# Optimization experiments

Measured on AMD Instinct MI355X. Metric: run time of the kernel, lower is better.

## Reference

```python
import jax, jax.numpy as jnp
import numpy as np

INPUT_SIZE = 2048
HIDDEN_SIZE = 2048
BATCH = 4096


def setup_inputs() -> dict:
    key = jax.random.key(0)
    ks = jax.random.split(key, 16)
    s_in = 1.0 / np.sqrt(INPUT_SIZE)
    s_h = 1.0 / np.sqrt(HIDDEN_SIZE)
    d = {
        "x": jax.random.normal(ks[0], (BATCH, INPUT_SIZE), jnp.float32),
        "h": jax.random.normal(ks[1], (BATCH, HIDDEN_SIZE), jnp.float32),
        "c": jax.random.normal(ks[2], (BATCH, HIDDEN_SIZE), jnp.float32),
    }
    # input-side weights [H, I] and biases (torch nn.Linear layout)
    for i, g in enumerate(["f", "i", "c", "o"]):
        d[f"W{g}x"] = jax.random.uniform(ks[3 + i], (HIDDEN_SIZE, INPUT_SIZE), jnp.float32, -s_in, s_in)
        d[f"b{g}x"] = jax.random.uniform(ks[7 + i], (HIDDEN_SIZE,), jnp.float32, -s_in, s_in)
        d[f"W{g}h"] = jax.random.uniform(ks[11 + i], (HIDDEN_SIZE, HIDDEN_SIZE), jnp.float32, -s_h, s_h)
    return d


def reference(x, h, c, Wfx, bfx, Wfh, Wix, bix, Wih, Wcx, bcx, Wch, Wox, box, Woh):
    # gate pre-activations: x @ W*x.T + b + h @ W*h.T
    f = jax.nn.relu(x @ Wfx.T + bfx + h @ Wfh.T)
    i = jax.nn.relu(x @ Wix.T + bix + h @ Wih.T)
    o = jax.nn.relu(x @ Wox.T + box + h @ Woh.T)
    c_tilde = jnp.tanh(x @ Wcx.T + bcx + h @ Wch.T)
    c_new = f * c + i * c_tilde
    h_new = o * jnp.tanh(c_new)
    return (h_new, c_new)
```

## Files before the change

kernel.cpp:

```cpp
#include <hip/hip_runtime.h>
#include <hip/hip_bf16.h>


#define HID 2048
#define BATCH_N 4096
#define KTOT 4096
#define BM 128
#define BN 64
#define BK 64
#define THREADS 256

typedef __attribute__((ext_vector_type(4))) float f32x4;
typedef __attribute__((ext_vector_type(8))) short bf16x8;

__device__ __forceinline__ short f2bf(float f) {
    union { float f; unsigned u; } v; v.f = f;
    unsigned r = v.u + 0x7FFFu + ((v.u >> 16) & 1u);
    return (short)(r >> 16);
}

__device__ __forceinline__ float fast_tanh(float v) {
    float e = __expf(2.0f * v);
    return 1.0f - 2.0f / (e + 1.0f);
}

__device__ __forceinline__ void gload_lds16(const short* g, short* l) {
    __builtin_amdgcn_global_load_lds(
        (const __attribute__((address_space(1))) unsigned int*)g,
        (__attribute__((address_space(3))) unsigned int*)l, 16, 0, 0);
}

struct CastParams {
    const float* x; const float* h;
    const float* Wx[4]; const float* Wh[4];
    short* A; short* B;
};

__global__ __launch_bounds__(256) void precast_kernel(CastParams q) {
    const long A_CH = (long)BATCH_N * (KTOT / 8);
    const long B_CH = 4L * HID * (KTOT / 8);
    const long total = A_CH + B_CH;
    for (long idx = (long)blockIdx.x * 256 + threadIdx.x; idx < total;
         idx += (long)gridDim.x * 256) {
        const float* src; short* dst; int row, k;
        if (idx < A_CH) {
            row = (int)(idx >> 9);
            k = (int)(idx & 511) << 3;
            src = (k < HID) ? &q.x[(size_t)row * HID + k]
                            : &q.h[(size_t)row * HID + (k - HID)];
            dst = &q.A[(size_t)row * KTOT];
        } else {
            long r = idx - A_CH;
            int g = (int)(r >> 20);
            int rem = (int)(r & ((1 << 20) - 1));
            row = rem >> 9;
            k = (rem & 511) << 3;
            src = (k < HID) ? &q.Wx[g][(size_t)row * HID + k]
                            : &q.Wh[g][(size_t)row * HID + (k - HID)];
            dst = &q.B[((size_t)g * HID + row) * KTOT];
        }
        float4 v0 = *(const float4*)src;
        float4 v1 = *(const float4*)(src + 4);
        int col = (k & ~63) | ((k & 63) ^ ((row & 7) << 3));
        bf16x8 s;
        s[0] = f2bf(v0.x); s[1] = f2bf(v0.y); s[2] = f2bf(v0.z); s[3] = f2bf(v0.w);
        s[4] = f2bf(v1.x); s[5] = f2bf(v1.y); s[6] = f2bf(v1.z); s[7] = f2bf(v1.w);
        *(bf16x8*)&dst[col] = s;
    }
}

struct GemmParams {
    const short* A; const short* B;
    const float* bx[4];
    const float* c;
    float* oh; float* oc;
};

__global__ __launch_bounds__(THREADS, 2) void gemm_lstm_kernel(GemmParams p) {
    __shared__ short sA[BM * BK];
    __shared__ short sB[4 * BN * BK];

    const int t = threadIdx.x;
    const int bm = blockIdx.x * BM;
    const int bn = blockIdx.y * BN;
    const int wave = t >> 6;
    const int lane = t & 63;
    const int wm = (wave >> 1) * 64;
    const int wn = (wave & 1) * 32;
    const int lr = lane & 15;
    const int lk = (lane >> 4) * 8;

    f32x4 acc[4][4][2];
    #pragma unroll
    for (int g = 0; g < 4; ++g)
        #pragma unroll
        for (int m = 0; m < 4; ++m)
            #pragma unroll
            for (int n = 0; n < 2; ++n)
                acc[g][m][n] = (f32x4){0.f, 0.f, 0.f, 0.f};

    const int srow = lane >> 3;
    const int kch = (lane & 7) * 8;
    const short* gA = p.A + (size_t)(bm + wave * 32 + srow) * KTOT + kch;
    const short* gB = p.B + ((size_t)wave * HID + bn + srow) * KTOT + kch;

    for (int k0 = 0; k0 < KTOT; k0 += BK) {
        #pragma unroll
        for (int j = 0; j < 4; ++j)
            gload_lds16(gA + (size_t)(j * 8) * KTOT + k0,
                        &sA[(wave * 32 + j * 8) * BK]);
        #pragma unroll
        for (int j = 0; j < 8; ++j)
            gload_lds16(gB + (size_t)(j * 8) * KTOT + k0,
                        &sB[(wave * 64 + j * 8) * BK]);

        __syncthreads();

        #pragma unroll
        for (int kk = 0; kk < 2; ++kk) {
            bf16x8 a[4];
            #pragma unroll
            for (int m = 0; m < 4; ++m) {
                int row = wm + m * 16 + lr;
                int kidx = (kk * 32 + lk) ^ ((row & 7) << 3);
                a[m] = *(const bf16x8*)&sA[row * BK + kidx];
            }
            #pragma unroll
            for (int g = 0; g < 4; ++g) {
                #pragma unroll
                for (int n = 0; n < 2; ++n) {
                    int brow = wn + n * 16 + lr;
                    int kidx = (kk * 32 + lk) ^ ((brow & 7) << 3);
                    bf16x8 b = *(const bf16x8*)&sB[(g * BN + brow) * BK + kidx];
                    #pragma unroll
                    for (int m = 0; m < 4; ++m)
                        acc[g][m][n] = __builtin_amdgcn_mfma_f32_16x16x32_bf16(
                            a[m], b, acc[g][m][n], 0, 0, 0);
                }
            }
        }

        __syncthreads();
    }

    float bias[4][2];
    #pragma unroll
    for (int g = 0; g < 4; ++g)
        #pragma unroll
        for (int n = 0; n < 2; ++n)
            bias[g][n] = p.bx[g][bn + wn + n * 16 + lr];

    #pragma unroll
    for (int m = 0; m < 4; ++m) {
        int rbase = bm + wm + m * 16 + (lane >> 4) * 4;
        #pragma unroll
        for (int r = 0; r < 4; ++r) {
            int row = rbase + r;
            #pragma unroll
            for (int n = 0; n < 2; ++n) {
                int col = bn + wn + n * 16 + lr;
                float pf = acc[0][m][n][r] + bias[0][n];
                float pi = acc[1][m][n][r] + bias[1][n];
                float pc = acc[2][m][n][r] + bias[2][n];
                float po = acc[3][m][n][r] + bias[3][n];
                float fg = fmaxf(pf, 0.f);
                float ig = fmaxf(pi, 0.f);
                float og = fmaxf(po, 0.f);
                float ct = fast_tanh(pc);
                float cv = p.c[(size_t)row * HID + col];
                float cn = fg * cv + ig * ct;
                float hn = og * fast_tanh(cn);
                p.oh[(size_t)row * HID + col] = hn;
                p.oc[(size_t)row * HID + col] = cn;
            }
        }
    }
}

struct Params {
    const float* x; const float* h; const float* c;
    const float* Wx[4]; const float* Wh[4]; const float* bx[4];
    float* oh; float* oc;
};

__global__ __launch_bounds__(THREADS, 2) void relulstm_fallback(Params p) {
    __shared__ short sA[BM * BK];
    __shared__ short sB[4][BN * BK];
    const int t = threadIdx.x;
    const int bm = blockIdx.x * BM;
    const int bn = blockIdx.y * BN;
    const int wave = t >> 6;
    const int lane = t & 63;
    const int wm = (wave >> 1) * 64;
    const int wn = (wave & 1) * 32;
    const int lr = lane & 15;
    const int lk = (lane >> 4) * 8;

    f32x4 acc[4][4][2];
    #pragma unroll
    for (int g = 0; g < 4; ++g)
        #pragma unroll
        for (int m = 0; m < 4; ++m)
            #pragma unroll
            for (int n = 0; n < 2; ++n)
                acc[g][m][n] = (f32x4){0.f, 0.f, 0.f, 0.f};

    for (int k0 = 0; k0 < 2 * HID; k0 += BK) {
        const bool xpart = (k0 < HID);
        const int kb = k0 & (HID - 1);
        const float* __restrict__ srcA = xpart ? p.x : p.h;
        #pragma unroll
        for (int i2 = 0; i2 < 8; ++i2) {
            int cidx = t + i2 * THREADS;
            int row = cidx >> 4;
            int kc = cidx & 15;
            float4 v = *(const float4*)&srcA[(size_t)(bm + row) * HID + kb + kc * 4];
            int idx = row * BK + ((kc * 4) ^ ((row & 7) << 3));
            short4 s;
            s.x = f2bf(v.x); s.y = f2bf(v.y); s.z = f2bf(v.z); s.w = f2bf(v.w);
            *(short4*)&sA[idx] = s;
        }
        #pragma unroll
        for (int i2 = 0; i2 < 16; ++i2) {
            const int g = i2 >> 2;
            int rem = t + (i2 & 3) * THREADS;
            int row = rem >> 4;
            int kc = rem & 15;
            const float* __restrict__ srcB = xpart ? p.Wx[g] : p.Wh[g];
            float4 v = *(const float4*)&srcB[(size_t)(bn + row) * HID + kb + kc * 4];
            int idx = row * BK + ((kc * 4) ^ ((row & 7) << 3));
            short4 s;
            s.x = f2bf(v.x); s.y = f2bf(v.y); s.z = f2bf(v.z); s.w = f2bf(v.w);
            *(short4*)&sB[g][idx] = s;
        }
        __syncthreads();
        #pragma unroll
        for (int kk = 0; kk < 2; ++kk) {
            bf16x8 a[4];
            #pragma unroll
            for (int m = 0; m < 4; ++m) {
                int row = wm + m * 16 + lr;
                int kidx = (kk * 32 + lk) ^ ((row & 7) << 3);
                a[m] = *(const bf16x8*)&sA[row * BK + kidx];
            }
            #pragma unroll
            for (int g = 0; g < 4; ++g) {
                #pragma unroll
                for (int n = 0; n < 2; ++n) {
                    int brow = wn + n * 16 + lr;
                    int kidx = (kk * 32 + lk) ^ ((brow & 7) << 3);
                    bf16x8 b = *(const bf16x8*)&sB[g][brow * BK + kidx];
                    #pragma unroll
                    for (int m = 0; m < 4; ++m)
                        acc[g][m][n] = __builtin_amdgcn_mfma_f32_16x16x32_bf16(
                            a[m], b, acc[g][m][n], 0, 0, 0);
                }
            }
        }
        __syncthreads();
    }

    float bias[4][2];
    #pragma unroll
    for (int g = 0; g < 4; ++g)
        #pragma unroll
        for (int n = 0; n < 2; ++n)
            bias[g][n] = p.bx[g][bn + wn + n * 16 + lr];

    #pragma unroll
    for (int m = 0; m < 4; ++m) {
        int rbase = bm + wm + m * 16 + (lane >> 4) * 4;
        #pragma unroll
        for (int r = 0; r < 4; ++r) {
            int row = rbase + r;
            #pragma unroll
            for (int n = 0; n < 2; ++n) {
                int col = bn + wn + n * 16 + lr;
                float pf = acc[0][m][n][r] + bias[0][n];
                float pi = acc[1][m][n][r] + bias[1][n];
                float pc = acc[2][m][n][r] + bias[2][n];
                float po = acc[3][m][n][r] + bias[3][n];
                float fg = fmaxf(pf, 0.f);
                float ig = fmaxf(pi, 0.f);
                float og = fmaxf(po, 0.f);
                float ct = fast_tanh(pc);
                float cv = p.c[(size_t)row * HID + col];
                float cn = fg * cv + ig * ct;
                float hn = og * fast_tanh(cn);
                p.oh[(size_t)row * HID + col] = hn;
                p.oc[(size_t)row * HID + col] = cn;
            }
        }
    }
}

extern "C" void kernel_launch(void* const* d_in, const int* in_sizes, int n_in,
                              void* d_out, int out_size, void* d_ws, size_t ws_size,
                              hipStream_t stream) {
    (void)in_sizes; (void)n_in; (void)out_size;
    const size_t A_BYTES = (size_t)BATCH_N * KTOT * 2;
    const size_t B_BYTES = (size_t)4 * HID * KTOT * 2;

    if (ws_size >= A_BYTES + B_BYTES) {
        short* A = (short*)d_ws;
        short* B = A + (size_t)BATCH_N * KTOT;

        CastParams q;
        q.x = (const float*)d_in[0];
        q.h = (const float*)d_in[1];
        for (int g = 0; g < 4; ++g) {
            q.Wx[g] = (const float*)d_in[3 + 3 * g];
            q.Wh[g] = (const float*)d_in[5 + 3 * g];
        }
        q.A = A; q.B = B;
        precast_kernel<<<2048, 256, 0, stream>>>(q);

        GemmParams p;
        p.A = A; p.B = B;
        p.c = (const float*)d_in[2];
        for (int g = 0; g < 4; ++g) p.bx[g] = (const float*)d_in[4 + 3 * g];
        p.oh = (float*)d_out;
        p.oc = (float*)d_out + (size_t)BATCH_N * HID;
        dim3 grid(BATCH_N / BM, HID / BN);
        gemm_lstm_kernel<<<grid, THREADS, 0, stream>>>(p);
    } else {
        Params p;
        p.x = (const float*)d_in[0];
        p.h = (const float*)d_in[1];
        p.c = (const float*)d_in[2];
        for (int g = 0; g < 4; ++g) {
            p.Wx[g] = (const float*)d_in[3 + 3 * g];
            p.bx[g] = (const float*)d_in[4 + 3 * g];
            p.Wh[g] = (const float*)d_in[5 + 3 * g];
        }
        p.oh = (float*)d_out;
        p.oc = (float*)d_out + (size_t)BATCH_N * HID;
        dim3 grid(BATCH_N / BM, HID / BN);
        relulstm_fallback<<<grid, THREADS, 0, stream>>>(p);
    }
}
```

Measured before the change: 318.9 us.

## Rewrite fused LSTM GEMM as 8-wave double-buffered, phase-interleaved pipeline

Replaces the 256-thread single-buffered GEMM with a 512-thread kernel computing a 256x64 tile per gate. LDS is double-buffered, and global-to-LDS loads for later K-chunks are interleaved across eight per-gate MFMA phases, with explicit vmcnt waits, barriers and setprio. The aim is to hide global load latency behind MFMA work and to reuse each B tile across more rows. In exchange it uses 64KB of LDS and carries high register pressure, which may limit occupancy, and the hand-scheduled barriers are fragile.

```diff
diff --git a/kernel.cpp b/kernel.cpp
--- a/kernel.cpp
+++ b/kernel.cpp
@@ -5,10 +5,7 @@
 #define HID 2048
 #define BATCH_N 4096
 #define KTOT 4096
-#define BM 128
-#define BN 64
 #define BK 64
-#define THREADS 256
 
 typedef __attribute__((ext_vector_type(4))) float f32x4;
 typedef __attribute__((ext_vector_type(8))) short bf16x8;
@@ -76,13 +73,157 @@
     float* oh; float* oc;
 };
 
-__global__ __launch_bounds__(THREADS, 2) void gemm_lstm_kernel(GemmParams p) {
-    __shared__ short sA[BM * BK];
-    __shared__ short sB[4 * BN * BK];
+__global__ __launch_bounds__(512, 2) void gemm_lstm_8ph(GemmParams p) {
+    __shared__ short sA[2][16384];
+    __shared__ short sB[2][16384];
 
     const int t = threadIdx.x;
-    const int bm = blockIdx.x * BM;
-    const int bn = blockIdx.y * BN;
+    const int wave = t >> 6;
+    const int lane = t & 63;
+    const int wr = wave >> 1;
+    const int wc = wave & 1;
+    const int lr = lane & 15;
+    const int lk = (lane >> 4) * 8;
+    const int sw = (lane & 7) << 3;
+    const int koff0 = lk ^ sw;
+    const int koff1 = (32 + lk) ^ sw;
+
+    const int bm = blockIdx.x * 256;
+    const int bn = blockIdx.y * 64;
+
+    const int aOff = (wr * 64 + lr) * 64;
+    const int bOff = (wc * 32 + lr) * 64;
+
+    const short* aSrc = p.A + (size_t)(bm + (t >> 3)) * KTOT + (t & 7) * 8;
+    const short* bSrc = p.B + (size_t)(bn + (t >> 3)) * KTOT + (t & 7) * 8;
+    const int ldsT = t * 8;
+
+    f32x4 acc[4][4][2];
+    #pragma unroll
+    for (int g = 0; g < 4; ++g)
+        #pragma unroll
+        for (int m = 0; m < 4; ++m)
+            #pragma unroll
+            for (int n = 0; n < 2; ++n)
+                acc[g][m][n] = (f32x4){0.f, 0.f, 0.f, 0.f};
+
+    bf16x8 a[4][2];
+    bf16x8 b[2][2];
+
+#define STAGE_A(bf, u, kp) gload_lds16(aSrc + (size_t)(u) * 64 * KTOT + (kp), \
+                                       &sA[bf][(u) * 4096 + ldsT])
+#define STAGE_B(bf, g, kp) gload_lds16(bSrc + (size_t)(g) * HID * KTOT + (kp), \
+                                       &sB[bf][(g) * 4096 + ldsT])
+#define READ_A(bf) do { _Pragma("unroll") for (int m = 0; m < 4; ++m) { \
+        a[m][0] = *(const bf16x8*)&sA[bf][aOff + m * 1024 + koff0]; \
+        a[m][1] = *(const bf16x8*)&sA[bf][aOff + m * 1024 + koff1]; } } while (0)
+#define READ_B(bf, g) do { _Pragma("unroll") for (int n = 0; n < 2; ++n) { \
+        b[n][0] = *(const bf16x8*)&sB[bf][(g) * 4096 + bOff + n * 1024 + koff0]; \
+        b[n][1] = *(const bf16x8*)&sB[bf][(g) * 4096 + bOff + n * 1024 + koff1]; } } while (0)
+#define MFMA_G(g) do { __builtin_amdgcn_s_setprio(1); \
+        _Pragma("unroll") for (int kk = 0; kk < 2; ++kk) \
+        _Pragma("unroll") for (int n = 0; n < 2; ++n) \
+        _Pragma("unroll") for (int m = 0; m < 4; ++m) \
+            acc[g][m][n] = __builtin_amdgcn_mfma_f32_16x16x32_bf16( \
+                a[m][kk], b[n][kk], acc[g][m][n], 0, 0, 0); \
+        __builtin_amdgcn_s_setprio(0); } while (0)
+#define BAR() __builtin_amdgcn_s_barrier()
+#define VMCNT6() asm volatile("s_waitcnt vmcnt(6)" ::: "memory")
+
+    STAGE_A(0, 0, 0); STAGE_A(0, 1, 0); STAGE_A(0, 2, 0); STAGE_A(0, 3, 0);
+    STAGE_B(0, 0, 0); STAGE_B(0, 1, 0); STAGE_B(0, 2, 0); STAGE_B(0, 3, 0);
+    STAGE_A(1, 0, BK); STAGE_A(1, 1, BK); STAGE_A(1, 2, BK); STAGE_A(1, 3, BK);
+    STAGE_B(1, 0, BK); STAGE_B(1, 1, BK);
+    VMCNT6();
+    BAR();
+
+    for (int it = 0; it < KTOT / (2 * BK); ++it) {
+        const int kc1 = ((2 * it + 1) * BK) & (KTOT - 1);
+        const int kc2 = ((2 * it + 2) * BK) & (KTOT - 1);
+        const int kc3 = ((2 * it + 3) * BK) & (KTOT - 1);
+
+        READ_A(0); READ_B(0, 0);
+        STAGE_B(1, 2, kc1); STAGE_B(1, 3, kc1);
+        BAR(); MFMA_G(0); BAR();
+        READ_B(0, 1);
+        STAGE_A(0, 0, kc2); STAGE_A(0, 1, kc2);
+        BAR(); MFMA_G(1); BAR();
+        READ_B(0, 2);
+        STAGE_A(0, 2, kc2); STAGE_A(0, 3, kc2);
+        BAR(); MFMA_G(2); BAR();
+        READ_B(0, 3);
+        STAGE_B(0, 0, kc2); STAGE_B(0, 1, kc2);
+        VMCNT6();
+        BAR(); MFMA_G(3); BAR();
+        READ_A(1); READ_B(1, 0);
+        STAGE_B(0, 2, kc2); STAGE_B(0, 3, kc2);
+        BAR(); MFMA_G(0); BAR();
+        READ_B(1, 1);
+        STAGE_A(1, 0, kc3); STAGE_A(1, 1, kc3);
+        BAR(); MFMA_G(1); BAR();
+        READ_B(1, 2);
+        STAGE_A(1, 2, kc3); STAGE_A(1, 3, kc3);
+        BAR(); MFMA_G(2); BAR();
+        READ_B(1, 3);
+        STAGE_B(1, 0, kc3); STAGE_B(1, 1, kc3);
+        VMCNT6();
+        BAR(); MFMA_G(3); BAR();
+    }
+    asm volatile("s_waitcnt vmcnt(0)" ::: "memory");
+
+    float bias[4][2];
+    #pragma unroll
+    for (int g = 0; g < 4; ++g)
+        #pragma unroll
+        for (int n = 0; n < 2; ++n)
+            bias[g][n] = p.bx[g][bn + wc * 32 + n * 16 + lr];
+
+    #pragma unroll
+    for (int m = 0; m < 4; ++m) {
+        int rbase = bm + wr * 64 + m * 16 + (lane >> 4) * 4;
+        #pragma unroll
+        for (int r = 0; r < 4; ++r) {
+            int row = rbase + r;
+            #pragma unroll
+            for (int n = 0; n < 2; ++n) {
+                int col = bn + wc * 32 + n * 16 + lr;
+                float pf = acc[0][m][n][r] + bias[0][n];
+                float pi = acc[1][m][n][r] + bias[1][n];
+                float pc = acc[2][m][n][r] + bias[2][n];
+                float po = acc[3][m][n][r] + bias[3][n];
+                float fg = fmaxf(pf, 0.f);
+                float ig = fmaxf(pi, 0.f);
+                float og = fmaxf(po, 0.f);
+                float ct = fast_tanh(pc);
+                float cv = p.c[(size_t)row * HID + col];
+                float cn = fg * cv + ig * ct;
+                float hn = og * fast_tanh(cn);
+                p.oh[(size_t)row * HID + col] = hn;
+                p.oc[(size_t)row * HID + col] = cn;
+            }
+        }
+    }
+#undef STAGE_A
+#undef STAGE_B
+#undef READ_A
+#undef READ_B
+#undef MFMA_G
+#undef BAR
+#undef VMCNT6
+}
+
+struct Params {
+    const float* x; const float* h; const float* c;
+    const float* Wx[4]; const float* Wh[4]; const float* bx[4];
+    float* oh; float* oc;
+};
+
+__global__ __launch_bounds__(256, 2) void relulstm_fallback(Params p) {
+    __shared__ short sA[128 * 64];
+    __shared__ short sB[4][64 * 64];
+    const int t = threadIdx.x;
+    const int bm = blockIdx.x * 128;
+    const int bn = blockIdx.y * 64;
     const int wave = t >> 6;
     const int lane = t & 63;
     const int wm = (wave >> 1) * 64;
@@ -99,23 +240,35 @@
             for (int n = 0; n < 2; ++n)
                 acc[g][m][n] = (f32x4){0.f, 0.f, 0.f, 0.f};
 
-    const int srow = lane >> 3;
-    const int kch = (lane & 7) * 8;
-    const short* gA = p.A + (size_t)(bm + wave * 32 + srow) * KTOT + kch;
-    const short* gB = p.B + ((size_t)wave * HID + bn + srow) * KTOT + kch;
-
-    for (int k0 = 0; k0 < KTOT; k0 += BK) {
-        #pragma unroll
-        for (int j = 0; j < 4; ++j)
-            gload_lds16(gA + (size_t)(j * 8) * KTOT + k0,
-                        &sA[(wave * 32 + j * 8) * BK]);
-        #pragma unroll
-        for (int j = 0; j < 8; ++j)
-            gload_lds16(gB + (size_t)(j * 8) * KTOT + k0,
-                        &sB[(wave * 64 + j * 8) * BK]);
-
+    for (int k0 = 0; k0 < 2 * HID; k0 += BK) {
+        const bool xpart = (k0 < HID);
+        const int kb = k0 & (HID - 1);
+        const float* __restrict__ srcA = xpart ? p.x : p.h;
+        #pragma unroll
+        for (int i2 = 0; i2 < 8; ++i2) {
+            int cidx = t + i2 * 256;
+            int row = cidx >> 4;
+            int kc = cidx & 15;
+            float4 v = *(const float4*)&srcA[(size_t)(bm + row) * HID + kb + kc * 4];
+            int idx = row * BK + ((kc * 4) ^ ((row & 7) << 3));
+            short4 s;
+            s.x = f2bf(v.x); s.y = f2bf(v.y); s.z = f2bf(v.z); s.w = f2bf(v.w);
+            *(short4*)&sA[idx] = s;
+        }
+        #pragma unroll
+        for (int i2 = 0; i2 < 16; ++i2) {
+            const int g = i2 >> 2;
+            int rem = t + (i2 & 3) * 256;
+            int row = rem >> 4;
+            int kc = rem & 15;
+            const float* __restrict__ srcB = xpart ? p.Wx[g] : p.Wh[g];
+            float4 v = *(const float4*)&srcB[(size_t)(bn + row) * HID + kb + kc * 4];
+            int idx = row * BK + ((kc * 4) ^ ((row & 7) << 3));
+            short4 s;
+            s.x = f2bf(v.x); s.y = f2bf(v.y); s.z = f2bf(v.z); s.w = f2bf(v.w);
+            *(short4*)&sB[g][idx] = s;
+        }
         __syncthreads();
-
         #pragma unroll
         for (int kk = 0; kk < 2; ++kk) {
             bf16x8 a[4];
@@ -131,7 +284,7 @@
                 for (int n = 0; n < 2; ++n) {
                     int brow = wn + n * 16 + lr;
                     int kidx = (kk * 32 + lk) ^ ((brow & 7) << 3);
-                    bf16x8 b = *(const bf16x8*)&sB[(g * BN + brow) * BK + kidx];
+                    bf16x8 b = *(const bf16x8*)&sB[g][brow * BK + kidx];
                     #pragma unroll
                     for (int m = 0; m < 4; ++m)
                         acc[g][m][n] = __builtin_amdgcn_mfma_f32_16x16x32_bf16(
@@ -139,7 +292,6 @@
                 }
             }
         }
-
         __syncthreads();
     }
 
@@ -177,123 +329,6 @@
     }
 }
 
-struct Params {
-    const float* x; const float* h; const float* c;
-    const float* Wx[4]; const float* Wh[4]; const float* bx[4];
-    float* oh; float* oc;
-};
-
-__global__ __launch_bounds__(THREADS, 2) void relulstm_fallback(Params p) {
-    __shared__ short sA[BM * BK];
-    __shared__ short sB[4][BN * BK];
-    const int t = threadIdx.x;
-    const int bm = blockIdx.x * BM;
-    const int bn = blockIdx.y * BN;
-    const int wave = t >> 6;
-    const int lane = t & 63;
-    const int wm = (wave >> 1) * 64;
-    const int wn = (wave & 1) * 32;
-    const int lr = lane & 15;
-    const int lk = (lane >> 4) * 8;
-
-    f32x4 acc[4][4][2];
-    #pragma unroll
-    for (int g = 0; g < 4; ++g)
-        #pragma unroll
-        for (int m = 0; m < 4; ++m)
-            #pragma unroll
-            for (int n = 0; n < 2; ++n)
-                acc[g][m][n] = (f32x4){0.f, 0.f, 0.f, 0.f};
-
-    for (int k0 = 0; k0 < 2 * HID; k0 += BK) {
-        const bool xpart = (k0 < HID);
-        const int kb = k0 & (HID - 1);
-        const float* __restrict__ srcA = xpart ? p.x : p.h;
-        #pragma unroll
-        for (int i2 = 0; i2 < 8; ++i2) {
-            int cidx = t + i2 * THREADS;
-            int row = cidx >> 4;
-            int kc = cidx & 15;
-            float4 v = *(const float4*)&srcA[(size_t)(bm + row) * HID + kb + kc * 4];
-            int idx = row * BK + ((kc * 4) ^ ((row & 7) << 3));
-            short4 s;
-            s.x = f2bf(v.x); s.y = f2bf(v.y); s.z = f2bf(v.z); s.w = f2bf(v.w);
-            *(short4*)&sA[idx] = s;
-        }
-        #pragma unroll
-        for (int i2 = 0; i2 < 16; ++i2) {
-            const int g = i2 >> 2;
-            int rem = t + (i2 & 3) * THREADS;
-            int row = rem >> 4;
-            int kc = rem & 15;
-            const float* __restrict__ srcB = xpart ? p.Wx[g] : p.Wh[g];
-            float4 v = *(const float4*)&srcB[(size_t)(bn + row) * HID + kb + kc * 4];
-            int idx = row * BK + ((kc * 4) ^ ((row & 7) << 3));
-            short4 s;
-            s.x = f2bf(v.x); s.y = f2bf(v.y); s.z = f2bf(v.z); s.w = f2bf(v.w);
-            *(short4*)&sB[g][idx] = s;
-        }
-        __syncthreads();
-        #pragma unroll
-        for (int kk = 0; kk < 2; ++kk) {
-            bf16x8 a[4];
-            #pragma unroll
-            for (int m = 0; m < 4; ++m) {
-                int row = wm + m * 16 + lr;
-                int kidx = (kk * 32 + lk) ^ ((row & 7) << 3);
-                a[m] = *(const bf16x8*)&sA[row * BK + kidx];
-            }
-            #pragma unroll
-            for (int g = 0; g < 4; ++g) {
-                #pragma unroll
-                for (int n = 0; n < 2; ++n) {
-                    int brow = wn + n * 16 + lr;
-                    int kidx = (kk * 32 + lk) ^ ((brow & 7) << 3);
-                    bf16x8 b = *(const bf16x8*)&sB[g][brow * BK + kidx];
-                    #pragma unroll
-                    for (int m = 0; m < 4; ++m)
-                        acc[g][m][n] = __builtin_amdgcn_mfma_f32_16x16x32_bf16(
-                            a[m], b, acc[g][m][n], 0, 0, 0);
-                }
-            }
-        }
-        __syncthreads();
-    }
-
-    float bias[4][2];
-    #pragma unroll
-    for (int g = 0; g < 4; ++g)
-        #pragma unroll
-        for (int n = 0; n < 2; ++n)
-            bias[g][n] = p.bx[g][bn + wn + n * 16 + lr];
-
-    #pragma unroll
-    for (int m = 0; m < 4; ++m) {
-        int rbase = bm + wm + m * 16 + (lane >> 4) * 4;
-        #pragma unroll
-        for (int r = 0; r < 4; ++r) {
-            int row = rbase + r;
-            #pragma unroll
-            for (int n = 0; n < 2; ++n) {
-                int col = bn + wn + n * 16 + lr;
-                float pf = acc[0][m][n][r] + bias[0][n];
-                float pi = acc[1][m][n][r] + bias[1][n];
-                float pc = acc[2][m][n][r] + bias[2][n];
-                float po = acc[3][m][n][r] + bias[3][n];
-                float fg = fmaxf(pf, 0.f);
-                float ig = fmaxf(pi, 0.f);
-                float og = fmaxf(po, 0.f);
-                float ct = fast_tanh(pc);
-                float cv = p.c[(size_t)row * HID + col];
-                float cn = fg * cv + ig * ct;
-                float hn = og * fast_tanh(cn);
-                p.oh[(size_t)row * HID + col] = hn;
-                p.oc[(size_t)row * HID + col] = cn;
-            }
-        }
-    }
-}
-
 extern "C" void kernel_launch(void* const* d_in, const int* in_sizes, int n_in,
                               void* d_out, int out_size, void* d_ws, size_t ws_size,
                               hipStream_t stream) {
@@ -321,8 +356,8 @@
         for (int g = 0; g < 4; ++g) p.bx[g] = (const float*)d_in[4 + 3 * g];
         p.oh = (float*)d_out;
         p.oc = (float*)d_out + (size_t)BATCH_N * HID;
-        dim3 grid(BATCH_N / BM, HID / BN);
-        gemm_lstm_kernel<<<grid, THREADS, 0, stream>>>(p);
+        dim3 grid(BATCH_N / 256, HID / 64);
+        gemm_lstm_8ph<<<grid, 512, 0, stream>>>(p);
     } else {
         Params p;
         p.x = (const float*)d_in[0];
@@ -335,7 +370,7 @@
         }
         p.oh = (float*)d_out;
         p.oc = (float*)d_out + (size_t)BATCH_N * HID;
-        dim3 grid(BATCH_N / BM, HID / BN);
-        relulstm_fallback<<<grid, THREADS, 0, stream>>>(p);
-    }
-}
+        dim3 grid(BATCH_N / 128, HID / 64);
+        relulstm_fallback<<<grid, 256, 0, stream>>>(p);
+    }
+}
```

Measured after the change: 317.4 us. About the same (-0.5%).

## Load A fragments directly from global into registers and remap block order

Applied to the files above, without the earlier changes.

The A operand tile is no longer staged in LDS. Each lane loads its MFMA A fragments straight from global memory into registers using a precomputed swizzled offset. The grid becomes 1D with a block-index remap that groups blocks in a way that may improve L2 reuse of A and B tiles. This saves LDS traffic and space for A, but A is now read redundantly by the waves that share rows, and the global loads may be less coalesced.

```diff
diff --git a/kernel.cpp b/kernel.cpp
--- a/kernel.cpp
+++ b/kernel.cpp
@@ -5,8 +5,6 @@
 #define HID 2048
 #define BATCH_N 4096
 #define KTOT 4096
-#define BM 128
-#define BN 64
 #define BK 64
 #define THREADS 256
 
@@ -76,19 +74,36 @@
     float* oh; float* oc;
 };
 
-__global__ __launch_bounds__(THREADS, 2) void gemm_lstm_kernel(GemmParams p) {
-    __shared__ short sA[BM * BK];
-    __shared__ short sB[4 * BN * BK];
+__global__ __launch_bounds__(THREADS, 2) void gemm_lstm_adir2(GemmParams p) {
+    __shared__ short sB[4 * 4096];
 
     const int t = threadIdx.x;
-    const int bm = blockIdx.x * BM;
-    const int bn = blockIdx.y * BN;
     const int wave = t >> 6;
     const int lane = t & 63;
     const int wm = (wave >> 1) * 64;
     const int wn = (wave & 1) * 32;
     const int lr = lane & 15;
     const int lk = (lane >> 4) * 8;
+    const int sw = (lane & 7) << 3;
+    const int koff0 = lk ^ sw;
+    const int koff1 = (32 + lk) ^ sw;
+
+    const int b0 = blockIdx.x;
+    const int nb = (b0 & 7) * 128 + (b0 >> 3);
+    const int bm = (nb >> 5) * 128;
+    const int bn = (nb & 31) * 64;
+
+    int voffA[4][2];
+    #pragma unroll
+    for (int m = 0; m < 4; ++m) {
+        int row = bm + wm + m * 16 + lr;
+        voffA[m][0] = row * KTOT + koff0;
+        voffA[m][1] = row * KTOT + koff1;
+    }
+
+    const int srow = lane >> 3;
+    const int kch = (lane & 7) * 8;
+    const short* gB = p.B + ((size_t)wave * HID + bn + srow) * KTOT + kch;
 
     f32x4 acc[4][4][2];
     #pragma unroll
@@ -99,43 +114,33 @@
             for (int n = 0; n < 2; ++n)
                 acc[g][m][n] = (f32x4){0.f, 0.f, 0.f, 0.f};
 
-    const int srow = lane >> 3;
-    const int kch = (lane & 7) * 8;
-    const short* gA = p.A + (size_t)(bm + wave * 32 + srow) * KTOT + kch;
-    const short* gB = p.B + ((size_t)wave * HID + bn + srow) * KTOT + kch;
+    bf16x8 a[4][2];
 
     for (int k0 = 0; k0 < KTOT; k0 += BK) {
-        #pragma unroll
-        for (int j = 0; j < 4; ++j)
-            gload_lds16(gA + (size_t)(j * 8) * KTOT + k0,
-                        &sA[(wave * 32 + j * 8) * BK]);
         #pragma unroll
         for (int j = 0; j < 8; ++j)
             gload_lds16(gB + (size_t)(j * 8) * KTOT + k0,
-                        &sB[(wave * 64 + j * 8) * BK]);
+                        &sB[wave * 4096 + j * 512]);
+        #pragma unroll
+        for (int m = 0; m < 4; ++m) {
+            a[m][0] = *(const bf16x8*)&p.A[voffA[m][0] + k0];
+            a[m][1] = *(const bf16x8*)&p.A[voffA[m][1] + k0];
+        }
 
         __syncthreads();
 
         #pragma unroll
         for (int kk = 0; kk < 2; ++kk) {
-            bf16x8 a[4];
-            #pragma unroll
-            for (int m = 0; m < 4; ++m) {
-                int row = wm + m * 16 + lr;
-                int kidx = (kk * 32 + lk) ^ ((row & 7) << 3);
-                a[m] = *(const bf16x8*)&sA[row * BK + kidx];
-            }
             #pragma unroll
             for (int g = 0; g < 4; ++g) {
                 #pragma unroll
                 for (int n = 0; n < 2; ++n) {
-                    int brow = wn + n * 16 + lr;
-                    int kidx = (kk * 32 + lk) ^ ((brow & 7) << 3);
-                    bf16x8 b = *(const bf16x8*)&sB[(g * BN + brow) * BK + kidx];
+                    bf16x8 b = *(const bf16x8*)&sB[g * 4096 +
+                        (wn + n * 16 + lr) * 64 + (kk ? koff1 : koff0)];
                     #pragma unroll
                     for (int m = 0; m < 4; ++m)
                         acc[g][m][n] = __builtin_amdgcn_mfma_f32_16x16x32_bf16(
-                            a[m], b, acc[g][m][n], 0, 0, 0);
+                            a[m][kk], b, acc[g][m][n], 0, 0, 0);
                 }
             }
         }
@@ -183,12 +188,12 @@
     float* oh; float* oc;
 };
 
-__global__ __launch_bounds__(THREADS, 2) void relulstm_fallback(Params p) {
-    __shared__ short sA[BM * BK];
-    __shared__ short sB[4][BN * BK];
+__global__ __launch_bounds__(256, 2) void relulstm_fallback(Params p) {
+    __shared__ short sA[128 * 64];
+    __shared__ short sB[4][64 * 64];
     const int t = threadIdx.x;
-    const int bm = blockIdx.x * BM;
-    const int bn = blockIdx.y * BN;
+    const int bm = blockIdx.x * 128;
+    const int bn = blockIdx.y * 64;
     const int wave = t >> 6;
     const int lane = t & 63;
     const int wm = (wave >> 1) * 64;
@@ -211,7 +216,7 @@
         const float* __restrict__ srcA = xpart ? p.x : p.h;
         #pragma unroll
         for (int i2 = 0; i2 < 8; ++i2) {
-            int cidx = t + i2 * THREADS;
+            int cidx = t + i2 * 256;
             int row = cidx >> 4;
             int kc = cidx & 15;
             float4 v = *(const float4*)&srcA[(size_t)(bm + row) * HID + kb + kc * 4];
@@ -223,7 +228,7 @@
         #pragma unroll
         for (int i2 = 0; i2 < 16; ++i2) {
             const int g = i2 >> 2;
-            int rem = t + (i2 & 3) * THREADS;
+            int rem = t + (i2 & 3) * 256;
             int row = rem >> 4;
             int kc = rem & 15;
             const float* __restrict__ srcB = xpart ? p.Wx[g] : p.Wh[g];
@@ -321,8 +326,7 @@
         for (int g = 0; g < 4; ++g) p.bx[g] = (const float*)d_in[4 + 3 * g];
         p.oh = (float*)d_out;
         p.oc = (float*)d_out + (size_t)BATCH_N * HID;
-        dim3 grid(BATCH_N / BM, HID / BN);
-        gemm_lstm_kernel<<<grid, THREADS, 0, stream>>>(p);
+        gemm_lstm_adir2<<<dim3(1024), THREADS, 0, stream>>>(p);
     } else {
         Params p;
         p.x = (const float*)d_in[0];
@@ -335,7 +339,7 @@
         }
         p.oh = (float*)d_out;
         p.oc = (float*)d_out + (size_t)BATCH_N * HID;
-        dim3 grid(BATCH_N / BM, HID / BN);
-        relulstm_fallback<<<grid, THREADS, 0, stream>>>(p);
-    }
-}
+        dim3 grid(BATCH_N / 128, HID / 64);
+        relulstm_fallback<<<grid, 256, 0, stream>>>(p);
+    }
+}
```

New measurement: 371.3 us. +16.4%, slower.
